# Kernel tuning notes

Measured on AMD Instinct MI355X. Metric: run time of the kernel, lower is better.

## Reference

```python
import jax, jax.numpy as jnp
import numpy as np
from jax import lax

B, N, K, L = 4, 5000, 16, 3
F, E, D, H = 2, 32, 64, 4
GRAPH_LAYERS = 2
FLOW_ITERS = 10
DUAL_ITERS = 10
DUAL_STEP = 0.01
DUAL_MOM = 0.9
BIG = 1e9


def setup_inputs() -> dict:
    key = jax.random.key(0)
    ks = jax.random.split(key, 32)
    p = lambda k, shape: jax.random.normal(k, shape, jnp.float32) * 0.1
    inp = {}
    inp['demands'] = jax.random.normal(ks[0], (B, N, 1), jnp.float32)
    inp['node_features'] = jax.random.uniform(ks[1], (B, N, F), jnp.float32)
    inp['edge_lengths'] = jax.random.uniform(ks[2], (B, N, K), jnp.float32, 0.5, 1.5)
    inp['embed_table'] = jax.random.normal(ks[3], (N, E), jnp.float32)
    inp['enc_W'] = p(ks[4], (E + F, D)); inp['enc_b'] = jnp.zeros((D,), jnp.float32)
    inp['nbW'] = p(ks[5], (D, D))
    inp['Wq'] = p(ks[6], (D, D)); inp['Wk'] = p(ks[7], (D, D))
    inp['Wv'] = p(ks[8], (D, D)); inp['Wo'] = p(ks[9], (D, D))
    inp['gWz'] = p(ks[10], (D, D)); inp['gUz'] = p(ks[11], (D, D)); inp['gbz'] = jnp.zeros((D,), jnp.float32)
    inp['gWr'] = p(ks[12], (D, D)); inp['gUr'] = p(ks[13], (D, D)); inp['gbr'] = jnp.zeros((D,), jnp.float32)
    inp['gWh'] = p(ks[14], (D, D)); inp['gUh'] = p(ks[15], (D, D)); inp['gbh'] = jnp.zeros((D,), jnp.float32)
    inp['dec_W1'] = p(ks[16], (2 * D, 32)); inp['dec_b1'] = jnp.zeros((32,), jnp.float32)
    inp['dec_W2'] = p(ks[17], (32, 1)); inp['dec_b2'] = jnp.zeros((1,), jnp.float32)
    inp['dual_W1'] = p(ks[18], (D, 32)); inp['dual_b1'] = jnp.zeros((32,), jnp.float32)
    inp['dual_W2'] = p(ks[19], (32, 1)); inp['dual_b2'] = jnp.zeros((1,), jnp.float32)
    inp['adj_lst'] = jax.random.randint(ks[20], (B, N, K), 0, N + 1, jnp.int32)
    inp['inv_adj_lst'] = jax.random.randint(ks[21], (B, N, K), 0, N + 1, jnp.int32)
    inp['neighborhoods'] = jax.random.randint(ks[22], (L, B, N, K), 0, N + 1, jnp.int32)
    perm = jax.vmap(lambda k: jax.random.permutation(k, N * K))(jax.random.split(ks[23], B)).astype(jnp.int32)
    inp['in_indices'] = perm                                   # edge slots regrouped by destination
    inp['rev_indices'] = jnp.argsort(perm, axis=1).astype(jnp.int32)  # inverse permutation
    inp['num_nodes'] = jnp.full((B,), N, jnp.int32)
    return inp


def _forward(demands, node_features, edge_lengths, embed_table, enc_W, enc_b, nbW,
             Wq, Wk, Wv, Wo, gWz, gUz, gbz, gWr, gUr, gbr, gWh, gUh, gbh,
             dec_W1, dec_b1, dec_W2, dec_b2, dual_W1, dual_b1, dual_W2, dual_b2,
             adj_lst, inv_adj_lst, neighborhoods, in_indices, rev_indices, num_nodes):
    dh = D // H
    # embedding lookup with max_norm=1 (rows clipped to unit norm)
    norms = jnp.linalg.norm(embed_table, axis=-1, keepdims=True)
    emb = embed_table / jnp.maximum(norms, 1.0)
    emb = jnp.broadcast_to(emb[None], (B, N, E))
    h = jnp.concatenate([emb, node_features], axis=-1) @ enc_W + enc_b  # [B,N,D]

    pad_idx = num_nodes[:, None, None]  # padding index == num_nodes

    def masked_gather(values, idx):
        # values [B,M,Dv], idx [B,N,K]; entries with idx == num_nodes gather zeros
        pad = jnp.concatenate([values, jnp.zeros_like(values[:, :1])], axis=1)
        g = jax.vmap(lambda v, i: v[i])(pad, idx)
        valid = (idx != pad_idx).astype(values.dtype)
        return g, valid

    for _ in range(GRAPH_LAYERS):
        hs = []
        for t in range(L):  # per-hop masked neighborhood aggregation
            nbr, valid = masked_gather(h, neighborhoods[t])       # [B,N,K,D]
            deg = jnp.maximum(valid.sum(-1, keepdims=True), 1.0)  # [B,N,1]
            hs.append(jnp.tanh((nbr.sum(axis=2) / deg) @ nbW))
        states = jnp.stack(hs, axis=2)                            # [B,N,L,D]
        q = (h @ Wq).reshape(B, N, H, dh)
        kk = (states @ Wk).reshape(B, N, L, H, dh)
        vv = (states @ Wv).reshape(B, N, L, H, dh)
        scores = jnp.einsum('bnhd,bnlhd->bnhl', q, kk) / np.float32(np.sqrt(dh))
        attn_weights = jax.nn.softmax(scores, axis=-1)            # [B,N,H,L]
        attn_out = jnp.einsum('bnhl,bnlhd->bnhd', attn_weights, vv).reshape(B, N, D)
        x = jnp.tanh(attn_out @ Wo)
        # GRU state update
        z = jax.nn.sigmoid(x @ gWz + h @ gUz + gbz)
        r = jax.nn.sigmoid(x @ gWr + h @ gUr + gbr)
        hh = jnp.tanh(x @ gWh + (r * h) @ gUh + gbh)
        h = (1.0 - z) * h + z * hh

    neighbor_states, _ = masked_gather(h, adj_lst)                # [B,N,K,D]
    mask = (adj_lst == pad_idx).astype(jnp.float32)
    adj_mask = 1.0 - mask
    tiled = adj_mask[..., None] * h[:, :, None, :]                # [B,N,K,D]
    concat = jnp.concatenate([jnp.broadcast_to(tiled, neighbor_states.shape), neighbor_states], axis=-1)
    node_weights = (jnp.tanh(concat @ dec_W1 + dec_b1) @ dec_W2 + dec_b2)[..., 0]  # [B,N,K]

    inv_mask = (inv_adj_lst == pad_idx).astype(jnp.float32)
    # destination attention: softmax over incoming edges grouped by destination, permuted back
    flat = node_weights.reshape(B, N * K)
    grouped = jnp.take_along_axis(flat, in_indices, axis=1).reshape(B, N, K)
    dest = jax.nn.softmax(grouped - BIG * inv_mask, axis=-1).reshape(B, N * K)
    node_weights = node_weights * jnp.take_along_axis(dest, rev_indices, axis=1).reshape(B, N, K)

    pred_weights = -BIG * mask + node_weights
    normalized_weights = jax.nn.softmax(pred_weights, axis=-1)

    # iterative proportional min-cost-flow solver
    supply = jax.nn.relu(-demands)  # [B,N,1]
    inv_valid = 1.0 - inv_mask
    def mcf_step(flow, _):
        inflow = jnp.take_along_axis(flow.reshape(B, N * K), in_indices, axis=1).reshape(B, N, K)
        inflow = (inflow * inv_valid).sum(-1, keepdims=True)
        return normalized_weights * (inflow + supply), None
    flow, _ = lax.scan(mcf_step, normalized_weights * supply, None, length=FLOW_ITERS)
    flow_cost = jnp.sum(edge_lengths * flow * flow, axis=(1, 2))  # quadratic edge cost

    # dual variables and dual flows via projected momentum descent
    dual_vars = jnp.tanh(h @ dual_W1 + dual_b1) @ dual_W2 + dual_b2   # [B,N,1]
    dual = adj_mask * dual_vars                                       # [B,N,K]
    dual_tr, _ = masked_gather(dual_vars, adj_lst)
    dual_diff = dual_tr[..., 0] - dual
    def dual_step(carry, _):
        f, acc = carry
        grad = 2.0 * edge_lengths * f + dual_diff
        acc = DUAL_MOM * acc + DUAL_STEP * grad
        f = jax.nn.relu(f - acc) * adj_mask
        return (f, acc), None
    (dual_flows, _), _ = lax.scan(dual_step, (jnp.zeros_like(dual_diff), jnp.zeros_like(dual_diff)), None, length=DUAL_ITERS)
    dual_demand = jnp.sum(dual_vars * demands, axis=(1, 2))
    dual_cost = jnp.sum(edge_lengths * dual_flows * dual_flows + dual_diff * dual_flows, axis=(1, 2)) - dual_demand
    return flow_cost - dual_cost  # per-graph primal-dual loss, shape [B]


def reference(demands, node_features, edge_lengths, embed_table, enc_W, enc_b, nbW,
              Wq, Wk, Wv, Wo, gWz, gUz, gbz, gWr, gUr, gbr, gWh, gUh, gbh,
              dec_W1, dec_b1, dec_W2, dec_b2, dual_W1, dual_b1, dual_W2, dual_b2,
              adj_lst, inv_adj_lst, neighborhoods, in_indices, rev_indices, num_nodes):
    return _forward(demands, node_features, edge_lengths, embed_table, enc_W, enc_b, nbW,
                    Wq, Wk, Wv, Wo, gWz, gUz, gbz, gWr, gUr, gbr, gWh, gUh, gbh,
                    dec_W1, dec_b1, dec_W2, dec_b2, dual_W1, dual_b1, dual_W2, dual_b2,
                    adj_lst, inv_adj_lst, neighborhoods, in_indices, rev_indices, num_nodes)
```

## Files before the change

kernel.cpp:

```cpp
#include <hip/hip_runtime.h>
#include <math.h>

#define B_ 4
#define N_ 5000
#define K_ 16
#define L_ 3
#define F_ 2
#define E_ 32
#define D_ 64
#define H_ 4
#define BN_ (B_*N_)
#define NK_ (N_*K_)
#define BIG_ 1.0e9f
#define RS_ 68

typedef __attribute__((ext_vector_type(8))) short s8v;
typedef __attribute__((ext_vector_type(4))) float f4v;

union FU { uint4 u; s8v s; };

__device__ __forceinline__ unsigned pack_bf16(float lo, float hi) {
    unsigned ul = __float_as_uint(lo);
    unsigned uh = __float_as_uint(hi);
    ul = (ul + 0x7fffu + ((ul >> 16) & 1u)) >> 16;
    uh = (uh + 0x7fffu + ((uh >> 16) & 1u)) & 0xffff0000u;
    return uh | ul;
}

__global__ __launch_bounds__(256) void k_prepW(
    const float* __restrict__ Wq, const float* __restrict__ nbW,
    const float* __restrict__ Wk, const float* __restrict__ Wv,
    const float* __restrict__ Wo,
    const float* __restrict__ gWz, const float* __restrict__ gUz,
    const float* __restrict__ gWr, const float* __restrict__ gUr,
    const float* __restrict__ gWh, const float* __restrict__ gUh,
    const float* __restrict__ decW1, unsigned* __restrict__ pf,
    float* __restrict__ acc)
{
    int m = blockIdx.x;
    if (m == 12) {
        if (threadIdx.x < 192) acc[threadIdx.x] = 0.f;
        return;
    }
    const float* src = nullptr;
    switch (m) {
        case 0: src = Wq;  break; case 1: src = nbW; break;
        case 2: src = Wk;  break; case 3: src = Wv;  break;
        case 4: src = Wo;  break; case 5: src = gWz; break;
        case 6: src = gUz; break; case 7: src = gWr; break;
        case 8: src = gUr; break; case 9: src = gWh; break;
        case 10: src = gUh; break; default: break;
    }
    for (int j = threadIdx.x; j < 2048; j += 256) {
        int fgrp = j >> 8;
        int li = j & 255;
        int e2 = li >> 6;
        int lane = li & 63;
        int s = fgrp >> 2, w = fgrp & 3;
        int k = 32 * s + 8 * (lane >> 4) + 2 * e2;
        int c = 16 * w + (lane & 15);
        float v0, v1;
        if (m < 11) {
            v0 = src[k * 64 + c];
            v1 = src[(k + 1) * 64 + c];
        } else {
            v0 = (c < 32) ? decW1[k * 32 + c]       : decW1[(64 + k) * 32 + (c - 32)];
            v1 = (c < 32) ? decW1[(k + 1) * 32 + c] : decW1[(64 + k + 1) * 32 + (c - 32)];
        }
        pf[m * 2048 + fgrp * 256 + lane * 4 + e2] = pack_bf16(v0, v1);
    }
}

__global__ __launch_bounds__(256) void k_encode(
    const float* __restrict__ embed, const float* __restrict__ feat,
    const float* __restrict__ encW, const float* __restrict__ encb,
    float* __restrict__ h)
{
    int wave = threadIdx.x >> 6;
    int lane = threadIdx.x & 63;
    int node = blockIdx.x * 4 + wave;
    int n = node % N_;

    float e = (lane < E_) ? embed[(size_t)n * E_ + lane] : 0.f;
    float ss = e * e;
    #pragma unroll
    for (int m = 32; m >= 1; m >>= 1) ss += __shfl_xor(ss, m, 64);
    float scale = 1.f / fmaxf(sqrtf(ss), 1.f);

    float inval = (lane < E_) ? e * scale
                : (lane < E_ + F_) ? feat[(size_t)node * F_ + (lane - E_)]
                : 0.f;

    float acc = encb[lane];
    #pragma unroll
    for (int i = 0; i < E_ + F_; ++i)
        acc = fmaf(__shfl(inval, i, 64), encW[i * D_ + lane], acc);
    h[(size_t)node * D_ + lane] = acc;
}

__device__ __forceinline__ s8v bfragG(const unsigned* __restrict__ pf,
                                      int m, int s, int w, int lane)
{
    FU f;
    f.u = *(const uint4*)&pf[m * 2048 + ((s * 4 + w) * 64 + lane) * 4];
    return f.s;
}

__device__ __forceinline__ s8v afragS(const float* T, int lane, int s)
{
    int row = lane & 15;
    int kb = 32 * s + 8 * (lane >> 4);
    float4 a = *(const float4*)&T[row * RS_ + kb];
    float4 b = *(const float4*)&T[row * RS_ + kb + 4];
    FU f;
    f.u.x = pack_bf16(a.x, a.y);
    f.u.y = pack_bf16(a.z, a.w);
    f.u.z = pack_bf16(b.x, b.y);
    f.u.w = pack_bf16(b.z, b.w);
    return f.s;
}

__device__ __forceinline__ void dwrite(float* T, int w, int lane, f4v d)
{
    int col = 16 * w + (lane & 15);
    int r0 = (lane >> 4) * 4;
    #pragma unroll
    for (int r = 0; r < 4; ++r) T[(r0 + r) * RS_ + col] = d[r];
}
__device__ __forceinline__ f4v dread(const float* T, int w, int lane)
{
    int col = 16 * w + (lane & 15);
    int r0 = (lane >> 4) * 4;
    f4v v;
    #pragma unroll
    for (int r = 0; r < 4; ++r) v[r] = T[(r0 + r) * RS_ + col];
    return v;
}

#define MFMA(a, b, c) __builtin_amdgcn_mfma_f32_16x16x32_bf16((a), (b), (c), 0, 0, 0)

__global__ __launch_bounds__(256, 5) void k_layer(
    const float* __restrict__ hin, float* __restrict__ hout,
    const int* __restrict__ neigh, const int* __restrict__ numn,
    const unsigned* __restrict__ pf,
    const float* __restrict__ gbz, const float* __restrict__ gbr,
    const float* __restrict__ gbh,
    float* __restrict__ Pout, int last)
{
    __shared__ __align__(16) float sM[3][16 * RS_];
    __shared__ __align__(16) float sH[16 * RS_];
    __shared__ __align__(16) float sX[16 * RS_];
    __shared__ int sIdx[3][256];

    int j = blockIdx.x;
    int xcd = j & 7, slot = j >> 3;
    int bb = xcd >> 1;
    int tile = slot * 2 + (xcd & 1);
    if (tile * 16 >= N_) return;

    int tx = threadIdx.x;
    int wv = tx >> 6, lane = tx & 63;
    int row = tx >> 4, cg = tx & 15, c0 = cg * 4;
    int ln = tile * 16 + row;
    bool act = ln < N_;
    int g = bb * N_ + (act ? ln : 0);
    int pad = numn[bb];
    const float4* hb4 = (const float4*)(hin + (size_t)bb * N_ * D_);

    float4 hld = act ? *(const float4*)&hin[(size_t)g * 64 + c0]
                     : make_float4(0.f, 0.f, 0.f, 0.f);
    *(float4*)&sH[row * RS_ + c0] = hld;
    #pragma unroll
    for (int t = 0; t < 3; ++t)
        sIdx[t][cg * 16 + row] = act ? neigh[((size_t)t * BN_ + g) * K_ + cg] : pad;
    __syncthreads();

    s8v hA0 = afragS(sH, lane, 0), hA1 = afragS(sH, lane, 1);
    f4v qD = {0.f, 0.f, 0.f, 0.f};
    qD = MFMA(hA0, bfragG(pf, 0, 0, wv, lane), qD);
    qD = MFMA(hA1, bfragG(pf, 0, 1, wv, lane), qD);

    #pragma unroll
    for (int t = 0; t < 3; ++t) {
        float4 s = make_float4(0.f, 0.f, 0.f, 0.f);
        int cnt = 0;
        #pragma unroll
        for (int k = 0; k < K_; ++k) {
            int idx = sIdx[t][k * 16 + row];
            if (idx != pad) {
                float4 v = hb4[(size_t)idx * 16 + cg];
                s.x += v.x; s.y += v.y; s.z += v.z; s.w += v.w;
                cnt++;
            }
        }
        float inv = 1.f / fmaxf((float)cnt, 1.f);
        *(float4*)&sM[t][row * RS_ + c0] =
            make_float4(s.x * inv, s.y * inv, s.z * inv, s.w * inv);
    }
    __syncthreads();

    s8v mA[3][2];
    #pragma unroll
    for (int t = 0; t < 3; ++t) {
        mA[t][0] = afragS(sM[t], lane, 0);
        mA[t][1] = afragS(sM[t], lane, 1);
    }
    __syncthreads();

    {
        s8v nB0 = bfragG(pf, 1, 0, wv, lane), nB1 = bfragG(pf, 1, 1, wv, lane);
        #pragma unroll
        for (int t = 0; t < 3; ++t) {
            f4v d = {0.f, 0.f, 0.f, 0.f};
            d = MFMA(mA[t][0], nB0, d);
            d = MFMA(mA[t][1], nB1, d);
            #pragma unroll
            for (int r = 0; r < 4; ++r) d[r] = tanhf(d[r]);
            dwrite(sM[t], wv, lane, d);
        }
    }
    __syncthreads();

    s8v stA[3][2];
    #pragma unroll
    for (int t = 0; t < 3; ++t) {
        stA[t][0] = afragS(sM[t], lane, 0);
        stA[t][1] = afragS(sM[t], lane, 1);
    }
    float sc[3][4];
    {
        s8v kB0 = bfragG(pf, 2, 0, wv, lane), kB1 = bfragG(pf, 2, 1, wv, lane);
        #pragma unroll
        for (int t = 0; t < 3; ++t) {
            f4v kk = {0.f, 0.f, 0.f, 0.f};
            kk = MFMA(stA[t][0], kB0, kk);
            kk = MFMA(stA[t][1], kB1, kk);
            float p0 = kk[0] * qD[0], p1 = kk[1] * qD[1];
            float p2 = kk[2] * qD[2], p3 = kk[3] * qD[3];
            #pragma unroll
            for (int m = 1; m < 16; m <<= 1) {
                p0 += __shfl_xor(p0, m, 64);
                p1 += __shfl_xor(p1, m, 64);
                p2 += __shfl_xor(p2, m, 64);
                p3 += __shfl_xor(p3, m, 64);
            }
            sc[t][0] = p0 * 0.25f; sc[t][1] = p1 * 0.25f;
            sc[t][2] = p2 * 0.25f; sc[t][3] = p3 * 0.25f;
        }
    }
    f4v w0v, w1v, w2v;
    #pragma unroll
    for (int r = 0; r < 4; ++r) {
        float p0 = sc[0][r], p1 = sc[1][r], p2 = sc[2][r];
        float mx = fmaxf(p0, fmaxf(p1, p2));
        float e0 = expf(p0 - mx), e1 = expf(p1 - mx), e2 = expf(p2 - mx);
        float inv = 1.f / (e0 + e1 + e2);
        w0v[r] = e0 * inv; w1v[r] = e1 * inv; w2v[r] = e2 * inv;
    }
    {
        s8v vB0 = bfragG(pf, 3, 0, wv, lane), vB1 = bfragG(pf, 3, 1, wv, lane);
        f4v vv0 = {0.f,0.f,0.f,0.f}, vv1 = {0.f,0.f,0.f,0.f}, vv2 = {0.f,0.f,0.f,0.f};
        vv0 = MFMA(stA[0][0], vB0, vv0); vv0 = MFMA(stA[0][1], vB1, vv0);
        vv1 = MFMA(stA[1][0], vB0, vv1); vv1 = MFMA(stA[1][1], vB1, vv1);
        vv2 = MFMA(stA[2][0], vB0, vv2); vv2 = MFMA(stA[2][1], vB1, vv2);
        f4v ao;
        #pragma unroll
        for (int r = 0; r < 4; ++r)
            ao[r] = w0v[r] * vv0[r] + w1v[r] * vv1[r] + w2v[r] * vv2[r];
        dwrite(sX, wv, lane, ao);
    }
    __syncthreads();

    s8v aoA0 = afragS(sX, lane, 0), aoA1 = afragS(sX, lane, 1);
    __syncthreads();

    {
        f4v xd = {0.f, 0.f, 0.f, 0.f};
        xd = MFMA(aoA0, bfragG(pf, 4, 0, wv, lane), xd);
        xd = MFMA(aoA1, bfragG(pf, 4, 1, wv, lane), xd);
        #pragma unroll
        for (int r = 0; r < 4; ++r) xd[r] = tanhf(xd[r]);
        dwrite(sX, wv, lane, xd);
    }
    __syncthreads();

    s8v xA0 = afragS(sX, lane, 0), xA1 = afragS(sX, lane, 1);
    f4v az = {0.f, 0.f, 0.f, 0.f}, ar = {0.f, 0.f, 0.f, 0.f};
    az = MFMA(xA0, bfragG(pf, 5, 0, wv, lane), az);
    az = MFMA(xA1, bfragG(pf, 5, 1, wv, lane), az);
    az = MFMA(hA0, bfragG(pf, 6, 0, wv, lane), az);
    az = MFMA(hA1, bfragG(pf, 6, 1, wv, lane), az);
    ar = MFMA(xA0, bfragG(pf, 7, 0, wv, lane), ar);
    ar = MFMA(xA1, bfragG(pf, 7, 1, wv, lane), ar);
    ar = MFMA(hA0, bfragG(pf, 8, 0, wv, lane), ar);
    ar = MFMA(hA1, bfragG(pf, 8, 1, wv, lane), ar);
    int col = 16 * wv + (lane & 15);
    float bzv = gbz[col], brv = gbr[col];
    f4v hD = dread(sH, wv, lane);
    f4v zg, rh;
    #pragma unroll
    for (int r = 0; r < 4; ++r) {
        zg[r] = 1.f / (1.f + expf(-(az[r] + bzv)));
        float rr = 1.f / (1.f + expf(-(ar[r] + brv)));
        rh[r] = rr * hD[r];
    }
    dwrite(sM[0], wv, lane, rh);
    __syncthreads();

    s8v rhA0 = afragS(sM[0], lane, 0), rhA1 = afragS(sM[0], lane, 1);
    f4v ah = {0.f, 0.f, 0.f, 0.f};
    ah = MFMA(xA0, bfragG(pf, 9, 0, wv, lane), ah);
    ah = MFMA(xA1, bfragG(pf, 9, 1, wv, lane), ah);
    ah = MFMA(rhA0, bfragG(pf, 10, 0, wv, lane), ah);
    ah = MFMA(rhA1, bfragG(pf, 10, 1, wv, lane), ah);
    float bhv = gbh[col];
    int lr0 = (lane >> 4) * 4;
    int nodeb = bb * N_ + tile * 16;
    f4v hp;
    #pragma unroll
    for (int r = 0; r < 4; ++r) {
        float hh = tanhf(ah[r] + bhv);
        hp[r] = (1.f - zg[r]) * hD[r] + zg[r] * hh;
        if (tile * 16 + lr0 + r < N_)
            hout[(size_t)(nodeb + lr0 + r) * 64 + col] = hp[r];
    }

    if (last) {
        dwrite(sX, wv, lane, hp);
        __syncthreads();
        s8v pA0 = afragS(sX, lane, 0), pA1 = afragS(sX, lane, 1);
        f4v pD = {0.f, 0.f, 0.f, 0.f};
        pD = MFMA(pA0, bfragG(pf, 11, 0, wv, lane), pD);
        pD = MFMA(pA1, bfragG(pf, 11, 1, wv, lane), pD);
        #pragma unroll
        for (int r = 0; r < 4; ++r)
            if (tile * 16 + lr0 + r < N_)
                Pout[(size_t)(nodeb + lr0 + r) * 64 + col] = pD[r];
    }
}

__global__ __launch_bounds__(256) void k_decoder2(
    const float* __restrict__ P, const int* __restrict__ adj,
    const float* __restrict__ b1, const float* __restrict__ W2,
    const float* __restrict__ b2, const int* __restrict__ num_nodes,
    float* __restrict__ nw)
{
    int j = blockIdx.x;
    int xcd = j & 7;
    int bb = xcd >> 1;
    int chunk = (j >> 3) * 2 + (xcd & 1);
    if (chunk >= 625) return;

    int half = threadIdx.x >> 5;
    int jj   = threadIdx.x & 31;
    float bias = b1[jj], w2 = W2[jj], b2v = b2[0];
    int pad = num_nodes[bb];
    const float* Pb = P + (size_t)bb * N_ * D_;

    #pragma unroll 1
    for (int p = 0; p < 16; ++p) {
        int le = chunk * 128 + p * 8 + half;
        size_t e = (size_t)bb * NK_ + le;
        int lnode = le >> 4;
        int a = adj[e];
        float own = Pb[(size_t)lnode * D_ + jj];
        bool pd = (a == pad);
        float nbr = pd ? 0.f : Pb[(size_t)(a == pad ? 0 : a) * D_ + 32 + jj];
        float am = pd ? 0.f : 1.f;
        float t = tanhf(bias + am * own + am * nbr);
        float part = t * w2;
        #pragma unroll
        for (int m = 1; m < 32; m <<= 1) part += __shfl_xor(part, m, 64);
        if (jj == 0) nw[e] = part + b2v;
    }
}

__global__ __launch_bounds__(256) void k_dualvars(
    const float* __restrict__ h, const float* __restrict__ W1,
    const float* __restrict__ b1, const float* __restrict__ W2,
    const float* __restrict__ b2, const float* __restrict__ demands,
    const int* __restrict__ num_nodes,
    float* __restrict__ dv, float* __restrict__ acc_out)
{
    __shared__ float sW1[D_ * 32];
    __shared__ float sW2[32];
    __shared__ float sPart[8];
    for (int i = threadIdx.x; i < D_ * 32; i += 256) sW1[i] = W1[i];
    if (threadIdx.x < 32) sW2[threadIdx.x] = W2[threadIdx.x];
    __syncthreads();

    int half = threadIdx.x >> 5;
    int j    = threadIdx.x & 31;
    int b = (blockIdx.x * 40) / N_;
    float bias = b1[j], b2v = b2[0];
    float local = 0.f;

    #pragma unroll 1
    for (int p = 0; p < 5; ++p) {
        int node = blockIdx.x * 40 + p * 8 + half;
        const float* hp = h + (size_t)node * D_;
        float h0 = hp[j], h1 = hp[j + 32];
        float acc = bias;
        #pragma unroll 8
        for (int i = 0; i < 32; ++i) {
            acc = fmaf(__shfl(h0, i, 32), sW1[i * 32 + j],        acc);
            acc = fmaf(__shfl(h1, i, 32), sW1[(i + 32) * 32 + j], acc);
        }
        float t = tanhf(acc);
        float part = t * sW2[j];
        #pragma unroll
        for (int m = 1; m < 32; m <<= 1) part += __shfl_xor(part, m, 64);
        if (j == 0) {
            float v = part + b2v;
            dv[node] = v;
            local += v * demands[node];
        }
    }
    if (j == 0) sPart[half] = local;
    __syncthreads();
    if (threadIdx.x == 0) {
        float s = 0.f;
        #pragma unroll
        for (int i = 0; i < 8; ++i) s += sPart[i];
        atomicAdd(&acc_out[(b * 3 + 2) * 16], s);
    }
}

__global__ void k_dest(
    const float* __restrict__ nw, const int* __restrict__ in_idx,
    const int* __restrict__ inv_adj, const int* __restrict__ num_nodes,
    float* __restrict__ dest)
{
    int j = blockIdx.x;
    int xcd = j & 7;
    int bb = xcd >> 1;
    int chunk = (j >> 3) * 2 + (xcd & 1);
    int ln = chunk * 256 + threadIdx.x;
    if (ln >= N_) return;
    int t = bb * N_ + ln;
    int pad = num_nodes[bb];
    float vals[K_]; float mx = -INFINITY;
    #pragma unroll
    for (int k = 0; k < K_; ++k) {
        int jj = in_idx[(size_t)t * K_ + k];
        float g = nw[(size_t)bb * NK_ + jj];
        float im = (inv_adj[(size_t)t * K_ + k] == pad) ? 1.f : 0.f;
        float v = g - BIG_ * im;
        vals[k] = v; mx = fmaxf(mx, v);
    }
    float s = 0.f;
    #pragma unroll
    for (int k = 0; k < K_; ++k) { vals[k] = expf(vals[k] - mx); s += vals[k]; }
    float invs = 1.f / s;
    #pragma unroll
    for (int k = 0; k < K_; ++k) dest[(size_t)t * K_ + k] = vals[k] * invs;
}

__global__ void k_normw(
    const float* __restrict__ nw, const float* __restrict__ dest,
    const int* __restrict__ rev, const int* __restrict__ adj,
    const int* __restrict__ num_nodes,
    float* __restrict__ normw)
{
    int j = blockIdx.x;
    int xcd = j & 7;
    int bb = xcd >> 1;
    int chunk = (j >> 3) * 2 + (xcd & 1);
    int ln = chunk * 256 + threadIdx.x;
    if (ln >= N_) return;
    int t = bb * N_ + ln;
    int pad = num_nodes[bb];
    float vals[K_]; float mx = -INFINITY;
    #pragma unroll
    for (int k = 0; k < K_; ++k) {
        size_t e = (size_t)t * K_ + k;
        float v = nw[e] * dest[(size_t)bb * NK_ + rev[e]];
        float m = (adj[e] == pad) ? 1.f : 0.f;
        v -= BIG_ * m;
        vals[k] = v; mx = fmaxf(mx, v);
    }
    float s = 0.f;
    #pragma unroll
    for (int k = 0; k < K_; ++k) { vals[k] = expf(vals[k] - mx); s += vals[k]; }
    float invs = 1.f / s;
    #pragma unroll
    for (int k = 0; k < K_; ++k)
        normw[(size_t)t * K_ + k] = vals[k] * invs;
}

__global__ void k_prep(
    const float* __restrict__ normw, const int* __restrict__ in_idx,
    const int* __restrict__ inv_adj, const int* __restrict__ num_nodes,
    const float* __restrict__ demands,
    float* __restrict__ supply, float* __restrict__ wgt, int* __restrict__ srcn,
    float* __restrict__ tot1)
{
    int j = blockIdx.x;
    int xcd = j & 7;
    int bb = xcd >> 1;
    int chunk = (j >> 3) * 2 + (xcd & 1);
    int ln = chunk * 256 + threadIdx.x;
    if (ln >= N_) return;
    int t = bb * N_ + ln;
    int pad = num_nodes[bb];
    float sup = fmaxf(-demands[t], 0.f);
    supply[t] = sup;
    float s1 = sup;
    #pragma unroll
    for (int k = 0; k < K_; ++k) {
        size_t e = (size_t)t * K_ + k;
        int jj = in_idx[e];
        bool valid = (inv_adj[e] != pad);
        float w = valid ? normw[(size_t)bb * NK_ + jj] : 0.f;
        int sn = bb * N_ + (jj >> 4);
        wgt[e] = w;
        srcn[e] = sn;
        s1 = fmaf(w, fmaxf(-demands[sn], 0.f), s1);
    }
    tot1[t] = s1;
}

__global__ void k_flowT(
    const float* __restrict__ totIn, const float* __restrict__ wgt,
    const int* __restrict__ srcn, const float* __restrict__ supply,
    float* __restrict__ totOut)
{
    int t = blockIdx.x * 256 + threadIdx.x;
    if (t >= BN_) return;
    float s = supply[t];
    #pragma unroll
    for (int k = 0; k < K_; ++k) {
        size_t e = (size_t)t * K_ + k;
        s = fmaf(wgt[e], totIn[srcn[e]], s);
    }
    totOut[t] = s;
}

__global__ __launch_bounds__(256) void k_dualred(
    const float* __restrict__ el, const float* __restrict__ dv,
    const int* __restrict__ adj, const int* __restrict__ num_nodes,
    const float* __restrict__ normw, const float* __restrict__ tot10,
    float* __restrict__ acc_out)
{
    int b = blockIdx.y;
    int ein = blockIdx.x * 256 + threadIdx.x;
    float c0 = 0.f, c1 = 0.f;
    if (ein < NK_) {
        size_t e = (size_t)b * NK_ + ein;
        int pad = num_nodes[b];
        int node = b * N_ + (ein >> 4);
        int a = adj[e];
        float am = (a == pad) ? 0.f : 1.f;
        float dtr = (a == pad) ? 0.f : dv[(size_t)b * N_ + a];
        float d = dtr - am * dv[node];
        float l = el[e];
        float f = 0.f, ac = 0.f;
        #pragma unroll
        for (int it = 0; it < 10; ++it) {
            float g = 2.f * l * f + d;
            ac = 0.9f * ac + 0.01f * g;
            f = fmaxf(f - ac, 0.f) * am;
        }
        float fl = normw[e] * tot10[node];
        c0 = l * fl * fl;
        c1 = l * f * f + d * f;
    }
    #pragma unroll
    for (int m = 1; m < 64; m <<= 1) { c0 += __shfl_xor(c0, m, 64); c1 += __shfl_xor(c1, m, 64); }
    __shared__ float s0[4], s1[4];
    int wave = threadIdx.x >> 6, lane = threadIdx.x & 63;
    if (lane == 0) { s0[wave] = c0; s1[wave] = c1; }
    __syncthreads();
    if (threadIdx.x == 0) {
        atomicAdd(&acc_out[(b * 3 + 0) * 16], s0[0] + s0[1] + s0[2] + s0[3]);
        atomicAdd(&acc_out[(b * 3 + 1) * 16], s1[0] + s1[1] + s1[2] + s1[3]);
    }
}

__global__ void k_final(const float* __restrict__ acc, float* __restrict__ out) {
    int b = threadIdx.x;
    if (b < B_)
        out[b] = acc[(b * 3 + 0) * 16] - acc[(b * 3 + 1) * 16] + acc[(b * 3 + 2) * 16];
}

extern "C" void kernel_launch(void* const* d_in, const int* in_sizes, int n_in,
                              void* d_out, int out_size, void* d_ws, size_t ws_size,
                              hipStream_t stream)
{
    const float* demands = (const float*)d_in[0];
    const float* feat    = (const float*)d_in[1];
    const float* el      = (const float*)d_in[2];
    const float* embed   = (const float*)d_in[3];
    const float* encW    = (const float*)d_in[4];
    const float* encb    = (const float*)d_in[5];
    const float* nbW     = (const float*)d_in[6];
    const float* Wq      = (const float*)d_in[7];
    const float* Wk      = (const float*)d_in[8];
    const float* Wv      = (const float*)d_in[9];
    const float* Wo      = (const float*)d_in[10];
    const float* gWz     = (const float*)d_in[11];
    const float* gUz     = (const float*)d_in[12];
    const float* gbz     = (const float*)d_in[13];
    const float* gWr     = (const float*)d_in[14];
    const float* gUr     = (const float*)d_in[15];
    const float* gbr     = (const float*)d_in[16];
    const float* gWh     = (const float*)d_in[17];
    const float* gUh     = (const float*)d_in[18];
    const float* gbh     = (const float*)d_in[19];
    const float* decW1   = (const float*)d_in[20];
    const float* decb1   = (const float*)d_in[21];
    const float* decW2   = (const float*)d_in[22];
    const float* decb2   = (const float*)d_in[23];
    const float* dualW1  = (const float*)d_in[24];
    const float* dualb1  = (const float*)d_in[25];
    const float* dualW2  = (const float*)d_in[26];
    const float* dualb2  = (const float*)d_in[27];
    const int* adj       = (const int*)d_in[28];
    const int* invadj    = (const int*)d_in[29];
    const int* neigh     = (const int*)d_in[30];
    const int* inidx     = (const int*)d_in[31];
    const int* revidx    = (const int*)d_in[32];
    const int* numn      = (const int*)d_in[33];

    float* ws     = (float*)d_ws;
    float* h0     = ws;
    float* h1     = ws + 1280000;
    float* nw     = ws + 2560000;
    float* dest   = ws + 2880000;
    float* normw  = ws + 3200000;
    float* wgt    = ws + 3520000;
    int*   srcn   = (int*)(ws + 3840000);
    float* totA   = ws + 4160000;
    float* totB   = ws + 4180000;
    float* supply = ws + 4200000;
    float* dv     = ws + 4220000;
    float* acc    = ws + 4240000;
    float* P      = ws + 4250000;
    unsigned* pf  = (unsigned*)(ws + 5540000);

    k_prepW<<<13, 256, 0, stream>>>(Wq, nbW, Wk, Wv, Wo, gWz, gUz, gWr, gUr,
                                    gWh, gUh, decW1, pf, acc);
    k_encode<<<BN_ / 4, 256, 0, stream>>>(embed, feat, encW, encb, h0);

    k_layer<<<1280, 256, 0, stream>>>(h0, h1, neigh, numn, pf,
                                      gbz, gbr, gbh, P, 0);
    k_layer<<<1280, 256, 0, stream>>>(h1, h0, neigh, numn, pf,
                                      gbz, gbr, gbh, P, 1);
    float* h = h0;

    k_decoder2<<<2504, 256, 0, stream>>>(P, adj, decb1, decW2, decb2, numn, nw);
    k_dualvars<<<BN_ / 40, 256, 0, stream>>>(h, dualW1, dualb1, dualW2, dualb2, demands, numn, dv, acc);
    k_dest<<<80, 256, 0, stream>>>(nw, inidx, invadj, numn, dest);
    k_normw<<<80, 256, 0, stream>>>(nw, dest, revidx, adj, numn, normw);
    k_prep<<<80, 256, 0, stream>>>(normw, inidx, invadj, numn, demands,
                                   supply, wgt, srcn, totA);

    float* cur = totA; float* nxt = totB;
    for (int it = 0; it < 9; ++it) {
        k_flowT<<<(BN_ + 255) / 256, 256, 0, stream>>>(cur, wgt, srcn, supply, nxt);
        float* tmp = cur; cur = nxt; nxt = tmp;
    }

    dim3 gred((NK_ + 255) / 256, B_);
    k_dualred<<<gred, 256, 0, stream>>>(el, dv, adj, numn, normw, cur, acc);
    k_final<<<1, 64, 0, stream>>>(acc, (float*)d_out);
}
```

Before: 178.7 us.

## Merge small launches and fold the last flow iteration into the dual reduction

Weight packing and the node encoder now run as one launch, and the decoder and dual-variable kernels are merged into a single grid that dispatches on block index. The final flow-propagation step is computed inside k_dualred with a 16-lane shuffle reduction over each node's edges, which removes one k_flowT launch. k_flowT also gets an XCD-aware block-to-graph mapping. The aim is to cut kernel-launch overhead and improve cache locality. The cost is some redundant gather work in the reduction and extra branching in the merged kernels.

```diff
diff --git a/kernel.cpp b/kernel.cpp
--- a/kernel.cpp
+++ b/kernel.cpp
@@ -27,7 +27,7 @@
     return uh | ul;
 }
 
-__global__ __launch_bounds__(256) void k_prepW(
+__global__ __launch_bounds__(256) void k_init(
     const float* __restrict__ Wq, const float* __restrict__ nbW,
     const float* __restrict__ Wk, const float* __restrict__ Wv,
     const float* __restrict__ Wo,
@@ -35,67 +35,66 @@
     const float* __restrict__ gWr, const float* __restrict__ gUr,
     const float* __restrict__ gWh, const float* __restrict__ gUh,
     const float* __restrict__ decW1, unsigned* __restrict__ pf,
-    float* __restrict__ acc)
+    float* __restrict__ acc,
+    const float* __restrict__ embed, const float* __restrict__ feat,
+    const float* __restrict__ encW, const float* __restrict__ encb,
+    float* __restrict__ h)
 {
     int m = blockIdx.x;
+    if (m < 12) {
+        const float* src = nullptr;
+        switch (m) {
+            case 0: src = Wq;  break; case 1: src = nbW; break;
+            case 2: src = Wk;  break; case 3: src = Wv;  break;
+            case 4: src = Wo;  break; case 5: src = gWz; break;
+            case 6: src = gUz; break; case 7: src = gWr; break;
+            case 8: src = gUr; break; case 9: src = gWh; break;
+            case 10: src = gUh; break; default: break;
+        }
+        for (int j = threadIdx.x; j < 2048; j += 256) {
+            int fgrp = j >> 8;
+            int li = j & 255;
+            int e2 = li >> 6;
+            int lane = li & 63;
+            int s = fgrp >> 2, w = fgrp & 3;
+            int k = 32 * s + 8 * (lane >> 4) + 2 * e2;
+            int c = 16 * w + (lane & 15);
+            float v0, v1;
+            if (m < 11) {
+                v0 = src[k * 64 + c];
+                v1 = src[(k + 1) * 64 + c];
+            } else {
+                v0 = (c < 32) ? decW1[k * 32 + c]       : decW1[(64 + k) * 32 + (c - 32)];
+                v1 = (c < 32) ? decW1[(k + 1) * 32 + c] : decW1[(64 + k + 1) * 32 + (c - 32)];
+            }
+            pf[m * 2048 + fgrp * 256 + lane * 4 + e2] = pack_bf16(v0, v1);
+        }
+        return;
+    }
     if (m == 12) {
         if (threadIdx.x < 192) acc[threadIdx.x] = 0.f;
         return;
     }
-    const float* src = nullptr;
-    switch (m) {
-        case 0: src = Wq;  break; case 1: src = nbW; break;
-        case 2: src = Wk;  break; case 3: src = Wv;  break;
-        case 4: src = Wo;  break; case 5: src = gWz; break;
-        case 6: src = gUz; break; case 7: src = gWr; break;
-        case 8: src = gUr; break; case 9: src = gWh; break;
-        case 10: src = gUh; break; default: break;
-    }
-    for (int j = threadIdx.x; j < 2048; j += 256) {
-        int fgrp = j >> 8;
-        int li = j & 255;
-        int e2 = li >> 6;
-        int lane = li & 63;
-        int s = fgrp >> 2, w = fgrp & 3;
-        int k = 32 * s + 8 * (lane >> 4) + 2 * e2;
-        int c = 16 * w + (lane & 15);
-        float v0, v1;
-        if (m < 11) {
-            v0 = src[k * 64 + c];
-            v1 = src[(k + 1) * 64 + c];
-        } else {
-            v0 = (c < 32) ? decW1[k * 32 + c]       : decW1[(64 + k) * 32 + (c - 32)];
-            v1 = (c < 32) ? decW1[(k + 1) * 32 + c] : decW1[(64 + k + 1) * 32 + (c - 32)];
-        }
-        pf[m * 2048 + fgrp * 256 + lane * 4 + e2] = pack_bf16(v0, v1);
-    }
-}
-
-__global__ __launch_bounds__(256) void k_encode(
-    const float* __restrict__ embed, const float* __restrict__ feat,
-    const float* __restrict__ encW, const float* __restrict__ encb,
-    float* __restrict__ h)
-{
     int wave = threadIdx.x >> 6;
     int lane = threadIdx.x & 63;
-    int node = blockIdx.x * 4 + wave;
+    int node = (m - 13) * 4 + wave;
     int n = node % N_;
 
     float e = (lane < E_) ? embed[(size_t)n * E_ + lane] : 0.f;
     float ss = e * e;
     #pragma unroll
-    for (int m = 32; m >= 1; m >>= 1) ss += __shfl_xor(ss, m, 64);
+    for (int mm = 32; mm >= 1; mm >>= 1) ss += __shfl_xor(ss, mm, 64);
     float scale = 1.f / fmaxf(sqrtf(ss), 1.f);
 
     float inval = (lane < E_) ? e * scale
                 : (lane < E_ + F_) ? feat[(size_t)node * F_ + (lane - E_)]
                 : 0.f;
 
-    float acc = encb[lane];
+    float a = encb[lane];
     #pragma unroll
     for (int i = 0; i < E_ + F_; ++i)
-        acc = fmaf(__shfl(inval, i, 64), encW[i * D_ + lane], acc);
-    h[(size_t)node * D_ + lane] = acc;
+        a = fmaf(__shfl(inval, i, 64), encW[i * D_ + lane], a);
+    h[(size_t)node * D_ + lane] = a;
 }
 
 __device__ __forceinline__ s8v bfragG(const unsigned* __restrict__ pf,
@@ -339,65 +338,66 @@
     }
 }
 
-__global__ __launch_bounds__(256) void k_decoder2(
+__global__ __launch_bounds__(256) void k_dec_dual(
     const float* __restrict__ P, const int* __restrict__ adj,
     const float* __restrict__ b1, const float* __restrict__ W2,
     const float* __restrict__ b2, const int* __restrict__ num_nodes,
-    float* __restrict__ nw)
-{
-    int j = blockIdx.x;
-    int xcd = j & 7;
-    int bb = xcd >> 1;
-    int chunk = (j >> 3) * 2 + (xcd & 1);
-    if (chunk >= 625) return;
-
-    int half = threadIdx.x >> 5;
-    int jj   = threadIdx.x & 31;
-    float bias = b1[jj], w2 = W2[jj], b2v = b2[0];
-    int pad = num_nodes[bb];
-    const float* Pb = P + (size_t)bb * N_ * D_;
-
-    #pragma unroll 1
-    for (int p = 0; p < 16; ++p) {
-        int le = chunk * 128 + p * 8 + half;
-        size_t e = (size_t)bb * NK_ + le;
-        int lnode = le >> 4;
-        int a = adj[e];
-        float own = Pb[(size_t)lnode * D_ + jj];
-        bool pd = (a == pad);
-        float nbr = pd ? 0.f : Pb[(size_t)(a == pad ? 0 : a) * D_ + 32 + jj];
-        float am = pd ? 0.f : 1.f;
-        float t = tanhf(bias + am * own + am * nbr);
-        float part = t * w2;
-        #pragma unroll
-        for (int m = 1; m < 32; m <<= 1) part += __shfl_xor(part, m, 64);
-        if (jj == 0) nw[e] = part + b2v;
-    }
-}
-
-__global__ __launch_bounds__(256) void k_dualvars(
-    const float* __restrict__ h, const float* __restrict__ W1,
-    const float* __restrict__ b1, const float* __restrict__ W2,
-    const float* __restrict__ b2, const float* __restrict__ demands,
-    const int* __restrict__ num_nodes,
+    float* __restrict__ nw,
+    const float* __restrict__ h, const float* __restrict__ dW1,
+    const float* __restrict__ db1, const float* __restrict__ dW2,
+    const float* __restrict__ db2, const float* __restrict__ demands,
     float* __restrict__ dv, float* __restrict__ acc_out)
 {
     __shared__ float sW1[D_ * 32];
     __shared__ float sW2[32];
     __shared__ float sPart[8];
-    for (int i = threadIdx.x; i < D_ * 32; i += 256) sW1[i] = W1[i];
-    if (threadIdx.x < 32) sW2[threadIdx.x] = W2[threadIdx.x];
+
+    int blk = blockIdx.x;
+    if (blk < 2504) {
+        int xcd = blk & 7;
+        int bb = xcd >> 1;
+        int chunk = (blk >> 3) * 2 + (xcd & 1);
+        if (chunk >= 625) return;
+
+        int half = threadIdx.x >> 5;
+        int jj   = threadIdx.x & 31;
+        float bias = b1[jj], w2 = W2[jj], b2v = b2[0];
+        int pad = num_nodes[bb];
+        const float* Pb = P + (size_t)bb * N_ * D_;
+
+        #pragma unroll 1
+        for (int p = 0; p < 16; ++p) {
+            int le = chunk * 128 + p * 8 + half;
+            size_t e = (size_t)bb * NK_ + le;
+            int lnode = le >> 4;
+            int a = adj[e];
+            float own = Pb[(size_t)lnode * D_ + jj];
+            bool pd = (a == pad);
+            float nbr = pd ? 0.f : Pb[(size_t)(a == pad ? 0 : a) * D_ + 32 + jj];
+            float am = pd ? 0.f : 1.f;
+            float t = tanhf(bias + am * own + am * nbr);
+            float part = t * w2;
+            #pragma unroll
+            for (int m = 1; m < 32; m <<= 1) part += __shfl_xor(part, m, 64);
+            if (jj == 0) nw[e] = part + b2v;
+        }
+        return;
+    }
+
+    int bid = blk - 2504;
+    for (int i = threadIdx.x; i < D_ * 32; i += 256) sW1[i] = dW1[i];
+    if (threadIdx.x < 32) sW2[threadIdx.x] = dW2[threadIdx.x];
     __syncthreads();
 
     int half = threadIdx.x >> 5;
     int j    = threadIdx.x & 31;
-    int b = (blockIdx.x * 40) / N_;
-    float bias = b1[j], b2v = b2[0];
+    int b = (bid * 40) / N_;
+    float bias = db1[j], b2v = db2[0];
     float local = 0.f;
 
     #pragma unroll 1
     for (int p = 0; p < 5; ++p) {
-        int node = blockIdx.x * 40 + p * 8 + half;
+        int node = bid * 40 + p * 8 + half;
         const float* hp = h + (size_t)node * D_;
         float h0 = hp[j], h1 = hp[j + 32];
         float acc = bias;
@@ -525,8 +525,13 @@
     const int* __restrict__ srcn, const float* __restrict__ supply,
     float* __restrict__ totOut)
 {
-    int t = blockIdx.x * 256 + threadIdx.x;
-    if (t >= BN_) return;
+    int j = blockIdx.x;
+    int xcd = j & 7;
+    int bb = xcd >> 1;
+    int chunk = (j >> 3) * 2 + (xcd & 1);
+    int ln = chunk * 256 + threadIdx.x;
+    if (ln >= N_) return;
+    int t = bb * N_ + ln;
     float s = supply[t];
     #pragma unroll
     for (int k = 0; k < K_; ++k) {
@@ -539,7 +544,9 @@
 __global__ __launch_bounds__(256) void k_dualred(
     const float* __restrict__ el, const float* __restrict__ dv,
     const int* __restrict__ adj, const int* __restrict__ num_nodes,
-    const float* __restrict__ normw, const float* __restrict__ tot10,
+    const float* __restrict__ normw,
+    const float* __restrict__ tot9, const float* __restrict__ wgt,
+    const int* __restrict__ srcn, const float* __restrict__ supply,
     float* __restrict__ acc_out)
 {
     int b = blockIdx.y;
@@ -561,7 +568,11 @@
             ac = 0.9f * ac + 0.01f * g;
             f = fmaxf(f - ac, 0.f) * am;
         }
-        float fl = normw[e] * tot10[node];
+        float part = wgt[e] * tot9[srcn[e]];
+        #pragma unroll
+        for (int m = 1; m < 16; m <<= 1) part += __shfl_xor(part, m, 64);
+        float tot10 = supply[node] + part;
+        float fl = normw[e] * tot10;
         c0 = l * fl * fl;
         c1 = l * f * f + d * f;
     }
@@ -638,9 +649,9 @@
     float* P      = ws + 4250000;
     unsigned* pf  = (unsigned*)(ws + 5540000);
 
-    k_prepW<<<13, 256, 0, stream>>>(Wq, nbW, Wk, Wv, Wo, gWz, gUz, gWr, gUr,
-                                    gWh, gUh, decW1, pf, acc);
-    k_encode<<<BN_ / 4, 256, 0, stream>>>(embed, feat, encW, encb, h0);
+    k_init<<<13 + BN_ / 4, 256, 0, stream>>>(Wq, nbW, Wk, Wv, Wo, gWz, gUz,
+                                             gWr, gUr, gWh, gUh, decW1, pf, acc,
+                                             embed, feat, encW, encb, h0);
 
     k_layer<<<1280, 256, 0, stream>>>(h0, h1, neigh, numn, pf,
                                       gbz, gbr, gbh, P, 0);
@@ -648,20 +659,22 @@
                                       gbz, gbr, gbh, P, 1);
     float* h = h0;
 
-    k_decoder2<<<2504, 256, 0, stream>>>(P, adj, decb1, decW2, decb2, numn, nw);
-    k_dualvars<<<BN_ / 40, 256, 0, stream>>>(h, dualW1, dualb1, dualW2, dualb2, demands, numn, dv, acc);
+    k_dec_dual<<<3004, 256, 0, stream>>>(P, adj, decb1, decW2, decb2, numn, nw,
+                                         h, dualW1, dualb1, dualW2, dualb2,
+                                         demands, dv, acc);
     k_dest<<<80, 256, 0, stream>>>(nw, inidx, invadj, numn, dest);
     k_normw<<<80, 256, 0, stream>>>(nw, dest, revidx, adj, numn, normw);
     k_prep<<<80, 256, 0, stream>>>(normw, inidx, invadj, numn, demands,
                                    supply, wgt, srcn, totA);
 
     float* cur = totA; float* nxt = totB;
-    for (int it = 0; it < 9; ++it) {
-        k_flowT<<<(BN_ + 255) / 256, 256, 0, stream>>>(cur, wgt, srcn, supply, nxt);
+    for (int it = 0; it < 8; ++it) {
+        k_flowT<<<80, 256, 0, stream>>>(cur, wgt, srcn, supply, nxt);
         float* tmp = cur; cur = nxt; nxt = tmp;
     }
 
     dim3 gred((NK_ + 255) / 256, B_);
-    k_dualred<<<gred, 256, 0, stream>>>(el, dv, adj, numn, normw, cur, acc);
+    k_dualred<<<gred, 256, 0, stream>>>(el, dv, adj, numn, normw,
+                                        cur, wgt, srcn, supply, acc);
     k_final<<<1, 64, 0, stream>>>(acc, (float*)d_out);
 }
```

New measurement: 170.9 us. 4.4% less time.
